# Optimization experiments

Hardware: AMD Instinct MI355X
Metric: run time of the kernel (lower is better)

Reference implementation:

```python
import jax, jax.numpy as jnp
import numpy as np

NUM_HEADS = 32
HEAD_DIM = 128
LORA_RANK = 512
Q_LORA_RANK = 1536
BSZ = 16
SEQ_LEN = 4096


def setup_inputs() -> dict:
    key = jax.random.key(0)
    k1, k2, k3, k4, k5, k6 = jax.random.split(key, 6)
    hd = NUM_HEADS * HEAD_DIM
    return {
        "hidden_states_q": jax.random.normal(k1, (BSZ, Q_LORA_RANK), dtype=jnp.float32),
        "compressed_kv": jax.random.normal(k2, (BSZ, SEQ_LEN, LORA_RANK), dtype=jnp.float32),
        # nn.Linear params: weight [out, in], bias [out]
        "Wq": jax.random.normal(k3, (hd, Q_LORA_RANK), dtype=jnp.float32) / np.sqrt(Q_LORA_RANK),
        "bq": jax.random.normal(k4, (hd,), dtype=jnp.float32) * 0.01,
        "Wkv": jax.random.normal(k5, (hd, LORA_RANK), dtype=jnp.float32) / np.sqrt(LORA_RANK),
        "bkv": jax.random.normal(k6, (hd,), dtype=jnp.float32) * 0.01,
    }


def reference(hidden_states_q, compressed_kv, Wq, bq, Wkv, bkv):
    bsz = hidden_states_q.shape[0]
    seq_len = compressed_kv.shape[1]
    # q: [b, h, d]
    q = (hidden_states_q @ Wq.T + bq).reshape(bsz, NUM_HEADS, HEAD_DIM)
    # kv decompression: [b, s, h, d] (same tensor used for both K and V)
    kv = (compressed_kv @ Wkv.T + bkv).reshape(bsz, seq_len, NUM_HEADS, HEAD_DIM)
    # attention scores per head over seq (note: original has NO 1/sqrt(d) scaling)
    attn = jnp.einsum('bhd,bshd->bhs', q, kv)
    attn = jax.nn.softmax(attn, axis=-1)
    out = jnp.einsum('bhs,bshd->bhd', attn, kv)
    return out.reshape(bsz, NUM_HEADS * HEAD_DIM)
```

## Files before the change

### kernel.cpp

```cpp
#include <hip/hip_runtime.h>

#define B  16
#define S  4096
#define R  512
#define QR 1536
#define H  32
#define D  128
#define HD 4096
#define SC 128
#define CH 32
#define KT 32
#define NT1 16

using f32x4 = __attribute__((ext_vector_type(4))) float;
using s16x8 = __attribute__((ext_vector_type(8))) short;
union bfu { s16x8 v; uint u[4]; };

typedef const void __attribute__((address_space(1)))* gas_t;
typedef void __attribute__((address_space(3)))* las_t;

__device__ __forceinline__ void gload16(const void* g, void* l) {
  __builtin_amdgcn_global_load_lds((gas_t)g, (las_t)l, 16, 0, 0);
}
__device__ __forceinline__ ushort bf_hi(float x) {
  return (ushort)(__float_as_uint(x) >> 16);
}
__device__ __forceinline__ float hi_f(float x) {
  return __uint_as_float(__float_as_uint(x) & 0xFFFF0000u);
}
__device__ __forceinline__ uint pack_hi2(float x, float y) {
  return (__float_as_uint(x) >> 16) | (__float_as_uint(y) & 0xFFFF0000u);
}
__device__ __forceinline__ ushort f2bf_rne(float x) {
  uint u = __float_as_uint(x);
  return (ushort)((u + 0x7FFFu + ((u >> 16) & 1u)) >> 16);
}
__device__ __forceinline__ float bf2f(ushort u) {
  return __uint_as_float((uint)u << 16);
}

__global__ __launch_bounds__(512) void k_q(const float* __restrict__ hsq,
                                           const float* __restrict__ Wq,
                                           const float* __restrict__ bq,
                                           float* __restrict__ q) {
  __shared__ float hs[B * QR];
  int tid = threadIdx.x;
  for (int idx = tid * 4; idx < B * QR; idx += 2048)
    *(float4*)&hs[idx] = *(const float4*)&hsq[idx];
  __syncthreads();

  int wave = tid >> 6, lane = tid & 63;
  int o = blockIdx.x * 16 + wave * 2;

  float acc0[B], acc1[B];
#pragma unroll
  for (int b = 0; b < B; ++b) { acc0[b] = 0.f; acc1[b] = 0.f; }

  const float* w0r = Wq + (size_t)o * QR;
  const float* w1r = w0r + QR;
  for (int k = lane * 4; k < QR; k += 256) {
    float4 wa = *(const float4*)&w0r[k];
    float4 wb = *(const float4*)&w1r[k];
#pragma unroll
    for (int b = 0; b < B; ++b) {
      float4 h4 = *(const float4*)&hs[b * QR + k];
      acc0[b] += wa.x * h4.x + wa.y * h4.y + wa.z * h4.z + wa.w * h4.w;
      acc1[b] += wb.x * h4.x + wb.y * h4.y + wb.z * h4.z + wb.w * h4.w;
    }
  }
#pragma unroll
  for (int b = 0; b < B; ++b) {
    float v0 = acc0[b], v1 = acc1[b];
#pragma unroll
    for (int off = 32; off > 0; off >>= 1) {
      v0 += __shfl_xor(v0, off);
      v1 += __shfl_xor(v1, off);
    }
    if (lane == 0) {
      q[b * HD + o]     = v0 + bq[o];
      q[b * HD + o + 1] = v1 + bq[o + 1];
    }
  }
}

__global__ __launch_bounds__(256) void k_qhat(const float* __restrict__ q,
                                              const float* __restrict__ Wkv,
                                              ushort* __restrict__ qhi,
                                              ushort* __restrict__ qlo) {
  int h = blockIdx.x;
  int r0 = blockIdx.y * 64;
  __shared__ float qs[B][D];
  int tid = threadIdx.x;
  for (int idx = tid; idx < B * D; idx += 256) {
    int b = idx >> 7, d = idx & (D - 1);
    qs[b][d] = q[b * HD + h * D + d];
  }
  __syncthreads();

  int r_l = tid & 63, bg = tid >> 6;
  float acc[4] = {0.f, 0.f, 0.f, 0.f};
  const float* wbase = Wkv + (size_t)(h * D) * R + r0 + r_l;
  for (int d = 0; d < D; d += 4) {
    float w0 = wbase[(d + 0) * R];
    float w1 = wbase[(d + 1) * R];
    float w2 = wbase[(d + 2) * R];
    float w3 = wbase[(d + 3) * R];
#pragma unroll
    for (int i = 0; i < 4; ++i) {
      float4 q4 = *(const float4*)&qs[bg * 4 + i][d];
      acc[i] += q4.x * w0 + q4.y * w1 + q4.z * w2 + q4.w * w3;
    }
  }
#pragma unroll
  for (int i = 0; i < 4; ++i) {
    size_t idx = ((size_t)(bg * 4 + i) * H + h) * R + r0 + r_l;
    qhi[idx] = bf_hi(acc[i]);
    qlo[idx] = bf_hi(acc[i] - hi_f(acc[i]));
  }
}

__global__ __launch_bounds__(512, 4) void k_fmha(const ushort* __restrict__ qhi,
                                                 const ushort* __restrict__ qlo,
                                                 const float* __restrict__ ckv,
                                                 ushort* __restrict__ part,
                                                 float* __restrict__ mbuf,
                                                 float* __restrict__ lbuf) {
  __shared__ __align__(16) float  csA[3][4096];
  __shared__ __align__(16) ushort qs[3][2048];
  __shared__ __align__(16) ushort Ps[H * 128];
  __shared__ float red[512];

  const int b = blockIdx.x, chunk = blockIdx.y;
  const int tid = threadIdx.x;
  const int lane = tid & 63, wv = tid >> 6;
  const int lcol = lane & 15, lgrp = lane >> 4;

  const float* cbase = ckv + ((size_t)b * S + (size_t)chunk * SC) * R;
  const ushort* qh_b = qhi + (size_t)b * H * R;
  const ushort* ql_b = qlo + (size_t)b * H * R;

  f32x4 acc[2];
  acc[0] = {0.f, 0.f, 0.f, 0.f};
  acc[1] = {0.f, 0.f, 0.f, 0.f};

  auto STAGE = [&](int bufsel, int kt) {
#pragma unroll
    for (int i = 0; i < 2; ++i) {
      int u = tid + 512 * i;
      int s = u >> 3;
      int jb = u & 7;
      int sb = jb ^ (s & 7);
      gload16(cbase + (size_t)s * R + kt + 4 * sb, &csA[bufsel][u * 4]);
    }
    if (tid < 256) {
      int h = tid >> 3;
      int jb = tid & 7;
      int lg = jb ^ (h & 7);
      const ushort* src = (lg < 4 ? qh_b : ql_b) + (size_t)h * R + kt + 8 * (lg & 3);
      gload16(src, &qs[bufsel][tid * 8]);
    }
  };

  auto COMPUTE = [&](int bufsel) {
    const int srow = 16 * wv + lcol;
    const int bkey = srow & 7;
    const float* brow = &csA[bufsel][srow * 32];
    float4 fa = *(const float4*)&brow[4 * ((2 * lgrp) ^ bkey)];
    float4 fb = *(const float4*)&brow[4 * ((2 * lgrp + 1) ^ bkey)];
    bfu bh, bl;
    bh.u[0] = pack_hi2(fa.x, fa.y); bh.u[1] = pack_hi2(fa.z, fa.w);
    bh.u[2] = pack_hi2(fb.x, fb.y); bh.u[3] = pack_hi2(fb.z, fb.w);
    bl.u[0] = pack_hi2(fa.x - hi_f(fa.x), fa.y - hi_f(fa.y));
    bl.u[1] = pack_hi2(fa.z - hi_f(fa.z), fa.w - hi_f(fa.w));
    bl.u[2] = pack_hi2(fb.x - hi_f(fb.x), fb.y - hi_f(fb.y));
    bl.u[3] = pack_hi2(fb.z - hi_f(fb.z), fb.w - hi_f(fb.w));
#pragma unroll
    for (int mt = 0; mt < 2; ++mt) {
      const int h = 16 * mt + lcol;
      const int hkey = h & 7;
      const ushort* qrow = &qs[bufsel][h * 64];
      s16x8 ah = *(const s16x8*)&qrow[8 * (lgrp ^ hkey)];
      s16x8 al = *(const s16x8*)&qrow[8 * ((4 + lgrp) ^ hkey)];
      acc[mt] = __builtin_amdgcn_mfma_f32_16x16x32_bf16(ah, bh.v, acc[mt], 0, 0, 0);
      acc[mt] = __builtin_amdgcn_mfma_f32_16x16x32_bf16(ah, bl.v, acc[mt], 0, 0, 0);
      acc[mt] = __builtin_amdgcn_mfma_f32_16x16x32_bf16(al, bh.v, acc[mt], 0, 0, 0);
    }
  };

  STAGE(0, 0);
  STAGE(1, KT);
#pragma unroll
  for (int t = 0; t < NT1; ++t) {
    if (t < NT1 - 1) {
      if (wv < 4) asm volatile("s_waitcnt vmcnt(3)" ::: "memory");
      else        asm volatile("s_waitcnt vmcnt(2)" ::: "memory");
    } else {
      asm volatile("s_waitcnt vmcnt(0)" ::: "memory");
    }
    __builtin_amdgcn_sched_barrier(0);
    __builtin_amdgcn_s_barrier();
    if (t + 2 < NT1) STAGE((t + 2) % 3, (t + 2) * KT);
    COMPUTE(t % 3);
  }

  float pm[2][4];
#pragma unroll
  for (int mt = 0; mt < 2; ++mt)
#pragma unroll
    for (int i = 0; i < 4; ++i) pm[mt][i] = acc[mt][i];
#pragma unroll
  for (int off = 1; off <= 8; off <<= 1)
#pragma unroll
    for (int mt = 0; mt < 2; ++mt)
#pragma unroll
      for (int i = 0; i < 4; ++i)
        pm[mt][i] = fmaxf(pm[mt][i], __shfl_xor(pm[mt][i], off));
  if (lcol == 0) {
#pragma unroll
    for (int mt = 0; mt < 2; ++mt)
#pragma unroll
      for (int i = 0; i < 4; ++i)
        red[(16 * mt + 4 * lgrp + i) * 8 + wv] = pm[mt][i];
  }
  __syncthreads();

  float e_[2][4], psum[2][4];
#pragma unroll
  for (int mt = 0; mt < 2; ++mt)
#pragma unroll
    for (int i = 0; i < 4; ++i) {
      int h = 16 * mt + 4 * lgrp + i;
      float4 r0 = *(float4*)&red[h * 8];
      float4 r1 = *(float4*)&red[h * 8 + 4];
      float m = fmaxf(fmaxf(fmaxf(r0.x, r0.y), fmaxf(r0.z, r0.w)),
                      fmaxf(fmaxf(r1.x, r1.y), fmaxf(r1.z, r1.w)));
      float e = __expf(acc[mt][i] - m);
      e_[mt][i] = e;
      psum[mt][i] = e;
    }
#pragma unroll
  for (int off = 1; off <= 8; off <<= 1)
#pragma unroll
    for (int mt = 0; mt < 2; ++mt)
#pragma unroll
      for (int i = 0; i < 4; ++i)
        psum[mt][i] += __shfl_xor(psum[mt][i], off);
  if (lcol == 0) {
#pragma unroll
    for (int mt = 0; mt < 2; ++mt)
#pragma unroll
      for (int i = 0; i < 4; ++i)
        red[256 + (16 * mt + 4 * lgrp + i) * 8 + wv] = psum[mt][i];
  }
#pragma unroll
  for (int mt = 0; mt < 2; ++mt)
#pragma unroll
    for (int i = 0; i < 4; ++i) {
      int h = 16 * mt + 4 * lgrp + i;
      int s = 16 * wv + lcol;
      Ps[h * 128 + (((s >> 3) ^ (h & 7)) << 3) + (s & 7)] = f2bf_rne(e_[mt][i]);
    }
  __syncthreads();

  if (wv == 0 && lcol == 0) {
#pragma unroll
    for (int mt = 0; mt < 2; ++mt)
#pragma unroll
      for (int i = 0; i < 4; ++i) {
        int h = 16 * mt + 4 * lgrp + i;
        float4 r0 = *(float4*)&red[h * 8];
        float4 r1 = *(float4*)&red[h * 8 + 4];
        float M = fmaxf(fmaxf(fmaxf(r0.x, r0.y), fmaxf(r0.z, r0.w)),
                        fmaxf(fmaxf(r1.x, r1.y), fmaxf(r1.z, r1.w)));
        float4 l0 = *(float4*)&red[256 + h * 8];
        float4 l1 = *(float4*)&red[256 + h * 8 + 4];
        float L = (l0.x + l0.y + l0.z + l0.w) + (l1.x + l1.y + l1.z + l1.w);
        mbuf[((size_t)b * CH + chunk) * H + h] = M;
        lbuf[((size_t)b * CH + chunk) * H + h] = L;
      }
  }

  const int nt = wv & 1, mtr = wv >> 1;
  s16x8 bp[4];
#pragma unroll
  for (int k4 = 0; k4 < 4; ++k4) {
    int h = 16 * nt + lcol;
    int kb = 4 * k4 + lgrp;
    bp[k4] = *(const s16x8*)&Ps[h * 128 + ((kb ^ (h & 7)) << 3)];
  }

  ushort* cs2 = (ushort*)&csA[0][0];
  const int sA = 16 * wv + 2 * (lane >> 4);
  const int r4 = 4 * lcol;
  float4 ve[2], vo[2];
  ushort* pb2 = part + (size_t)(b * CH + chunk) * H * R;

  auto LOAD2 = [&](int rt) {
    const float* basE = cbase + (size_t)sA * R + rt * 64 + r4;
#pragma unroll
    for (int jj = 0; jj < 2; ++jj) {
      const float* p = basE + (size_t)(8 * jj) * R;
      ve[jj] = *(const float4*)p;
      vo[jj] = *(const float4*)(p + R);
    }
  };
  auto WRITE2 = [&](int bufsel) {
    ushort* t2 = cs2 + bufsel * 8192;
    const int soff = sA & 7;
#pragma unroll
    for (int jj = 0; jj < 2; ++jj) {
      const int sblk = 2 * wv + jj;
      float fe[4] = {ve[jj].x, ve[jj].y, ve[jj].z, ve[jj].w};
      float fo[4] = {vo[jj].x, vo[jj].y, vo[jj].z, vo[jj].w};
#pragma unroll
      for (int i = 0; i < 4; ++i) {
        int r = r4 + i;
        *(uint*)&t2[r * 128 + 8 * (sblk ^ (r & 7)) + soff] = pack_hi2(fe[i], fo[i]);
      }
    }
  };
  auto COMPUTE2 = [&](int bufsel, int rt) {
    const ushort* t2 = cs2 + bufsel * 8192;
    const int rl = 16 * mtr + lcol;
    const int rk = rl & 7;
    f32x4 a2 = {0.f, 0.f, 0.f, 0.f};
#pragma unroll
    for (int k4 = 0; k4 < 4; ++k4) {
      s16x8 av = *(const s16x8*)&t2[(size_t)rl * 128 + 8 * ((4 * k4 + lgrp) ^ rk)];
      a2 = __builtin_amdgcn_mfma_f32_16x16x32_bf16(av, bp[k4], a2, 0, 0, 0);
    }
    uint2 w2;
    w2.x = pack_hi2(a2[0], a2[1]);
    w2.y = pack_hi2(a2[2], a2[3]);
    const int rg = rt * 64 + 16 * mtr + 4 * lgrp;
    *(uint2*)&pb2[(size_t)(16 * nt + lcol) * R + rg] = w2;
  };

  LOAD2(0);
  WRITE2(0);
  __syncthreads();
#pragma unroll
  for (int rt = 0; rt < 8; ++rt) {
    if (rt < 7) LOAD2(rt + 1);
    COMPUTE2(rt & 1, rt);
    if (rt < 7) WRITE2((rt + 1) & 1);
    __syncthreads();
  }
}

__global__ __launch_bounds__(256) void k_combine(const ushort* __restrict__ part,
                                                 const float* __restrict__ mbuf,
                                                 const float* __restrict__ lbuf,
                                                 float* __restrict__ ctx) {
  const int bid = blockIdx.x;
  const int b = bid >> 5, h = bid & 31;
  const int tid = threadIdx.x;
  float mv[CH], wv[CH];
  float M = -3.0e38f;
#pragma unroll
  for (int c = 0; c < CH; ++c) {
    mv[c] = mbuf[((size_t)b * CH + c) * H + h];
    M = fmaxf(M, mv[c]);
  }
  float denom = 0.f;
#pragma unroll
  for (int c = 0; c < CH; ++c) {
    wv[c] = __expf(mv[c] - M);
    denom += wv[c] * lbuf[((size_t)b * CH + c) * H + h];
  }
  const float inv = 1.f / denom;
  float s0 = 0.f, s1 = 0.f;
#pragma unroll
  for (int c = 0; c < CH; ++c) {
    const ushort* pp = part + (((size_t)b * CH + c) * H + h) * R;
    uint u = *(const uint*)&pp[2 * tid];
    s0 += wv[c] * bf2f((ushort)(u & 0xFFFFu));
    s1 += wv[c] * bf2f((ushort)(u >> 16));
  }
  float2 o2 = {s0 * inv, s1 * inv};
  *(float2*)&ctx[((size_t)b * H + h) * R + 2 * tid] = o2;
}

__global__ __launch_bounds__(256) void k_out(const float* __restrict__ ctx,
                                             const float* __restrict__ Wkv,
                                             const float* __restrict__ bkv,
                                             float* __restrict__ out) {
  int h = blockIdx.x;
  int d0 = blockIdx.y * 32;
  __shared__ float cs[B][R];
  int tid = threadIdx.x;
  for (int idx = tid * 4; idx < B * R; idx += 1024) {
    int b = idx >> 9, r = idx & 511;
    *(float4*)&cs[b][r] = *(const float4*)&ctx[(size_t)(b * H + h) * R + r];
  }
  __syncthreads();

  int dg = tid & 31;
  int bg = tid >> 5;
  int d = d0 + dg;
  int b0 = bg * 2;
  float acc0 = 0.f, acc1 = 0.f;
  const float* wrow = Wkv + ((size_t)(h * D + d)) * R;
  for (int i = 0; i < R; i += 4) {
    float4 w4 = *(const float4*)&wrow[i];
    float4 ca = *(const float4*)&cs[b0][i];
    float4 cb = *(const float4*)&cs[b0 + 1][i];
    acc0 += w4.x * ca.x + w4.y * ca.y + w4.z * ca.z + w4.w * ca.w;
    acc1 += w4.x * cb.x + w4.y * cb.y + w4.z * cb.z + w4.w * cb.w;
  }
  float bv = bkv[h * D + d];
  out[(size_t)b0 * HD + h * D + d]       = acc0 + bv;
  out[(size_t)(b0 + 1) * HD + h * D + d] = acc1 + bv;
}

extern "C" void kernel_launch(void* const* d_in, const int* in_sizes, int n_in,
                              void* d_out, int out_size, void* d_ws, size_t ws_size,
                              hipStream_t stream) {
  (void)in_sizes; (void)n_in; (void)out_size; (void)ws_size;
  const float* hsq = (const float*)d_in[0];
  const float* ckv = (const float*)d_in[1];
  const float* Wq  = (const float*)d_in[2];
  const float* bq  = (const float*)d_in[3];
  const float* Wkv = (const float*)d_in[4];
  const float* bkv = (const float*)d_in[5];
  float* out = (float*)d_out;

  float* ws   = (float*)d_ws;
  float* q    = ws;
  float* ctx  = q + 65536;
  float* mbuf = ctx + 262144;
  float* lbuf = mbuf + 16384;
  ushort* qhi  = (ushort*)(lbuf + 16384);
  ushort* qlo  = qhi + 262144;
  ushort* part = qlo + 262144;

  k_q<<<256, 512, 0, stream>>>(hsq, Wq, bq, q);
  k_qhat<<<dim3(32, 8), 256, 0, stream>>>(q, Wkv, qhi, qlo);
  k_fmha<<<dim3(B, CH), 512, 0, stream>>>(qhi, qlo, ckv, part, mbuf, lbuf);
  k_combine<<<B * H, 256, 0, stream>>>(part, mbuf, lbuf, ctx);
  k_out<<<dim3(32, 4), 256, 0, stream>>>(ctx, Wkv, bkv, out);
}
```

Before: 92.47 us.

## Widen score-phase K tile to 128 and replace triple buffering with synced single buffer

Raises the score-phase K tile from 32 to 128 columns, so the loop runs 4 steps instead of 16. The triple-buffered async staging with hand-tuned vmcnt waits is replaced by a single LDS buffer, fenced by __syncthreads before and after each compute step. Fewer, larger steps cut per-iteration barrier and loop overhead and give more MFMA work per step. In exchange, global-to-LDS loads no longer overlap compute, and the larger LDS footprint (lower launch-bounds occupancy hint) may leave fewer resident blocks per CU.

```diff
diff --git a/kernel.cpp b/kernel.cpp
--- a/kernel.cpp
+++ b/kernel.cpp
@@ -9,8 +9,8 @@
 #define HD 4096
 #define SC 128
 #define CH 32
-#define KT 32
-#define NT1 16
+#define KT 128
+#define NT1 4
 
 using f32x4 = __attribute__((ext_vector_type(4))) float;
 using s16x8 = __attribute__((ext_vector_type(8))) short;
@@ -119,14 +119,14 @@
   }
 }
 
-__global__ __launch_bounds__(512, 4) void k_fmha(const ushort* __restrict__ qhi,
+__global__ __launch_bounds__(512, 2) void k_fmha(const ushort* __restrict__ qhi,
                                                  const ushort* __restrict__ qlo,
                                                  const float* __restrict__ ckv,
                                                  ushort* __restrict__ part,
                                                  float* __restrict__ mbuf,
                                                  float* __restrict__ lbuf) {
-  __shared__ __align__(16) float  csA[3][4096];
-  __shared__ __align__(16) ushort qs[3][2048];
+  __shared__ __align__(16) float  csA[SC * KT];
+  __shared__ __align__(16) ushort qs[H * 256];
   __shared__ __align__(16) ushort Ps[H * 128];
   __shared__ float red[512];
 
@@ -143,64 +143,65 @@
   acc[0] = {0.f, 0.f, 0.f, 0.f};
   acc[1] = {0.f, 0.f, 0.f, 0.f};
 
-  auto STAGE = [&](int bufsel, int kt) {
+  auto STAGE = [&](int kt) {
+#pragma unroll
+    for (int i = 0; i < 8; ++i) {
+      int u = tid + 512 * i;
+      int s = u >> 5;
+      int jb = u & 31;
+      int sb = jb ^ (s & 7);
+      gload16(cbase + (size_t)s * R + kt + 4 * sb, &csA[u * 4]);
+    }
 #pragma unroll
     for (int i = 0; i < 2; ++i) {
       int u = tid + 512 * i;
-      int s = u >> 3;
-      int jb = u & 7;
-      int sb = jb ^ (s & 7);
-      gload16(cbase + (size_t)s * R + kt + 4 * sb, &csA[bufsel][u * 4]);
-    }
-    if (tid < 256) {
-      int h = tid >> 3;
-      int jb = tid & 7;
+      int h = u >> 5;
+      int jb = u & 31;
       int lg = jb ^ (h & 7);
-      const ushort* src = (lg < 4 ? qh_b : ql_b) + (size_t)h * R + kt + 8 * (lg & 3);
-      gload16(src, &qs[bufsel][tid * 8]);
+      const ushort* src = (lg < 16)
+          ? (qh_b + (size_t)h * R + kt + 8 * lg)
+          : (ql_b + (size_t)h * R + kt + 8 * (lg - 16));
+      gload16(src, &qs[u * 8]);
     }
   };
 
-  auto COMPUTE = [&](int bufsel) {
+  auto COMPUTE = [&]() {
     const int srow = 16 * wv + lcol;
     const int bkey = srow & 7;
-    const float* brow = &csA[bufsel][srow * 32];
-    float4 fa = *(const float4*)&brow[4 * ((2 * lgrp) ^ bkey)];
-    float4 fb = *(const float4*)&brow[4 * ((2 * lgrp + 1) ^ bkey)];
-    bfu bh, bl;
-    bh.u[0] = pack_hi2(fa.x, fa.y); bh.u[1] = pack_hi2(fa.z, fa.w);
-    bh.u[2] = pack_hi2(fb.x, fb.y); bh.u[3] = pack_hi2(fb.z, fb.w);
-    bl.u[0] = pack_hi2(fa.x - hi_f(fa.x), fa.y - hi_f(fa.y));
-    bl.u[1] = pack_hi2(fa.z - hi_f(fa.z), fa.w - hi_f(fa.w));
-    bl.u[2] = pack_hi2(fb.x - hi_f(fb.x), fb.y - hi_f(fb.y));
-    bl.u[3] = pack_hi2(fb.z - hi_f(fb.z), fb.w - hi_f(fb.w));
-#pragma unroll
-    for (int mt = 0; mt < 2; ++mt) {
-      const int h = 16 * mt + lcol;
-      const int hkey = h & 7;
-      const ushort* qrow = &qs[bufsel][h * 64];
-      s16x8 ah = *(const s16x8*)&qrow[8 * (lgrp ^ hkey)];
-      s16x8 al = *(const s16x8*)&qrow[8 * ((4 + lgrp) ^ hkey)];
-      acc[mt] = __builtin_amdgcn_mfma_f32_16x16x32_bf16(ah, bh.v, acc[mt], 0, 0, 0);
-      acc[mt] = __builtin_amdgcn_mfma_f32_16x16x32_bf16(ah, bl.v, acc[mt], 0, 0, 0);
-      acc[mt] = __builtin_amdgcn_mfma_f32_16x16x32_bf16(al, bh.v, acc[mt], 0, 0, 0);
+    const float* brow = &csA[srow * KT];
+#pragma unroll
+    for (int ks = 0; ks < 4; ++ks) {
+      const int lb0 = 8 * ks + 2 * lgrp;
+      float4 fa = *(const float4*)&brow[4 * (lb0 ^ bkey)];
+      float4 fb = *(const float4*)&brow[4 * ((lb0 + 1) ^ bkey)];
+      bfu bh, bl;
+      bh.u[0] = pack_hi2(fa.x, fa.y); bh.u[1] = pack_hi2(fa.z, fa.w);
+      bh.u[2] = pack_hi2(fb.x, fb.y); bh.u[3] = pack_hi2(fb.z, fb.w);
+      bl.u[0] = pack_hi2(fa.x - hi_f(fa.x), fa.y - hi_f(fa.y));
+      bl.u[1] = pack_hi2(fa.z - hi_f(fa.z), fa.w - hi_f(fa.w));
+      bl.u[2] = pack_hi2(fb.x - hi_f(fb.x), fb.y - hi_f(fb.y));
+      bl.u[3] = pack_hi2(fb.z - hi_f(fb.z), fb.w - hi_f(fb.w));
+#pragma unroll
+      for (int mt = 0; mt < 2; ++mt) {
+        const int h = 16 * mt + lcol;
+        const int hkey = h & 7;
+        const ushort* qrow = &qs[h * 256];
+        const int ablk = (4 * ks + lgrp) ^ hkey;
+        s16x8 ah = *(const s16x8*)&qrow[8 * ablk];
+        s16x8 al = *(const s16x8*)&qrow[128 + 8 * ablk];
+        acc[mt] = __builtin_amdgcn_mfma_f32_16x16x32_bf16(ah, bh.v, acc[mt], 0, 0, 0);
+        acc[mt] = __builtin_amdgcn_mfma_f32_16x16x32_bf16(ah, bl.v, acc[mt], 0, 0, 0);
+        acc[mt] = __builtin_amdgcn_mfma_f32_16x16x32_bf16(al, bh.v, acc[mt], 0, 0, 0);
+      }
     }
   };
 
-  STAGE(0, 0);
-  STAGE(1, KT);
 #pragma unroll
   for (int t = 0; t < NT1; ++t) {
-    if (t < NT1 - 1) {
-      if (wv < 4) asm volatile("s_waitcnt vmcnt(3)" ::: "memory");
-      else        asm volatile("s_waitcnt vmcnt(2)" ::: "memory");
-    } else {
-      asm volatile("s_waitcnt vmcnt(0)" ::: "memory");
-    }
-    __builtin_amdgcn_sched_barrier(0);
-    __builtin_amdgcn_s_barrier();
-    if (t + 2 < NT1) STAGE((t + 2) % 3, (t + 2) * KT);
-    COMPUTE(t % 3);
+    STAGE(t * KT);
+    __syncthreads();
+    COMPUTE();
+    __syncthreads();
   }
 
   float pm[2][4];
@@ -289,7 +290,7 @@
     bp[k4] = *(const s16x8*)&Ps[h * 128 + ((kb ^ (h & 7)) << 3)];
   }
 
-  ushort* cs2 = (ushort*)&csA[0][0];
+  ushort* cs2 = (ushort*)&csA[0];
   const int sA = 16 * wv + 2 * (lane >> 4);
   const int r4 = 4 * lcol;
   float4 ve[2], vo[2];
```

Result: slower. 101.0 us (+9.2%).
